# Optimization experiments

Measured on AMD Instinct MI355X. Metric: run time of the kernel, lower is better.

## Reference

```python
import jax, jax.numpy as jnp
import numpy as np


def setup_inputs() -> dict:
    key = jax.random.key(0)
    k1, k2, k3, k4, k5 = jax.random.split(key, 5)
    B, H, W, C, F = 8, 64, 64, 256, 64
    # glorot_uniform for 1x1 conv kernels [1,1,Cin,Cout]
    def glorot(k, cin, cout):
        lim = float(np.sqrt(6.0 / (cin + cout)))
        return jax.random.uniform(k, (1, 1, cin, cout), jnp.float32, -lim, lim)
    x = jax.random.normal(k1, (B, H, W, C), dtype=jnp.float32)
    Wf = glorot(k2, C, F)
    Wg = glorot(k3, C, F)
    Wh = glorot(k4, C, C)
    Wv = glorot(k5, C, C)
    gamma = jnp.zeros((1,), dtype=jnp.float32) + 0.1  # nonzero so attention path matters
    return {"x": x, "Wf": Wf, "Wg": Wg, "Wh": Wh, "Wv": Wv, "gamma": gamma}


def reference(x, Wf, Wg, Wh, Wv, gamma):
    B, H, W, C = x.shape
    N = H * W
    # 1x1 convs are pointwise matmuls over channels
    f = jnp.einsum('bhwc,cf->bhwf', x, Wf[0, 0])   # [B,H,W,F]
    g = jnp.einsum('bhwc,cf->bhwf', x, Wg[0, 0])   # [B,H,W,F]
    h = jnp.einsum('bhwc,cd->bhwd', x, Wh[0, 0])   # [B,H,W,C]
    ff = f.reshape(B, N, -1)                        # [B,N,F]
    gf = g.reshape(B, N, -1)                        # [B,N,F]
    hf = h.reshape(B, N, C)                         # [B,N,C]
    # s[b,i,j] = ff[b,i,:] . gf[b,j,:]  (no 1/sqrt(d) scaling, as in source)
    s = jnp.einsum('bif,bjf->bij', ff, gf)          # [B,N,N]
    beta = jax.nn.softmax(s, axis=-1)
    o = jnp.einsum('bij,bjc->bic', beta, hf)        # [B,N,C]
    o = o.reshape(B, H, W, C)
    o = jnp.einsum('bhwc,cd->bhwd', o, Wv[0, 0])
    return gamma * o + x
```

## Files before the change

kernel.cpp:

```cpp
#include <hip/hip_runtime.h>

typedef _Float16 half8   __attribute__((ext_vector_type(8)));
typedef _Float16 half4_t __attribute__((ext_vector_type(4)));
typedef float    float4_t __attribute__((ext_vector_type(4)));

#define B_   8
#define N_   4096
#define C_   256
#define F_   64
#define NROW (B_ * N_)
#define OPHALF ((size_t)NROW * C_)

#if defined(__has_builtin) && __has_builtin(__builtin_amdgcn_exp2f)
#define EXP2(x) __builtin_amdgcn_exp2f(x)
#else
#define EXP2(x) exp2f(x)
#endif
#define LOG2E 1.44269504f

static __device__ __forceinline__ float4_t mfma16(half8 a, half8 b, float4_t c) {
  return __builtin_amdgcn_mfma_f32_16x16x32_f16(a, b, c, 0, 0, 0);
}

template <int CTRL>
static __device__ __forceinline__ float dpp_f(float x) {
  return __int_as_float(__builtin_amdgcn_update_dpp(
      __float_as_int(x), __float_as_int(x), CTRL, 0xF, 0xF, false));
}
static __device__ __forceinline__ float row_max16(float v) {
  v = fmaxf(v, dpp_f<0x128>(v));
  v = fmaxf(v, dpp_f<0x124>(v));
  v = fmaxf(v, dpp_f<0x122>(v));
  v = fmaxf(v, dpp_f<0x121>(v));
  return v;
}
static __device__ __forceinline__ float row_sum16(float v) {
  v += dpp_f<0x128>(v);
  v += dpp_f<0x124>(v);
  v += dpp_f<0x122>(v);
  v += dpp_f<0x121>(v);
  return v;
}

__global__ __launch_bounds__(256) void prep_whvt(const float* __restrict__ Wh,
                                                 const float* __restrict__ Wv,
                                                 _Float16* __restrict__ whvt) {
  int d = blockIdx.x;
  int c = threadIdx.x;
  const float4_t* whr = (const float4_t*)(Wh + (size_t)c * 256);
  float acc = 0.f;
#pragma unroll 8
  for (int e4 = 0; e4 < 64; ++e4) {
    float4_t w4 = whr[e4];
    acc += w4[0] * Wv[(e4 * 4 + 0) * 256 + d];
    acc += w4[1] * Wv[(e4 * 4 + 1) * 256 + d];
    acc += w4[2] * Wv[(e4 * 4 + 2) * 256 + d];
    acc += w4[3] * Wv[(e4 * 4 + 3) * 256 + d];
  }
  whvt[d * 256 + c] = (_Float16)acc;
}

__global__ __launch_bounds__(256) void prep_wfgt(const float* __restrict__ Wf,
                                                 const float* __restrict__ Wg,
                                                 _Float16* __restrict__ wfgt) {
  int n = blockIdx.x;
  int c = threadIdx.x;
  float v = (n < 64) ? Wf[c * 64 + n] * LOG2E : Wg[c * 64 + (n - 64)];
  wfgt[n * 256 + c] = (_Float16)v;
}

__global__ __launch_bounds__(256) void transpose_x(const float* __restrict__ x,
                                                   _Float16* __restrict__ xT) {
  __shared__ float tile[32][33];
  int b  = blockIdx.x >> 7;
  int n0 = (blockIdx.x & 127) << 5;
  int c0 = blockIdx.y << 5;
  int tid = threadIdx.x;
  int r  = tid >> 3;
  int cc = (tid & 7) << 2;
  const float* src = x + ((size_t)(b * N_ + n0 + r)) * C_ + c0 + cc;
  float4_t v = *(const float4_t*)src;
  tile[r][cc + 0] = v[0]; tile[r][cc + 1] = v[1];
  tile[r][cc + 2] = v[2]; tile[r][cc + 3] = v[3];
  __syncthreads();
  half4_t o;
  o[0] = (_Float16)tile[cc + 0][r];
  o[1] = (_Float16)tile[cc + 1][r];
  o[2] = (_Float16)tile[cc + 2][r];
  o[3] = (_Float16)tile[cc + 3][r];
  _Float16* dst = xT + ((size_t)(b * C_ + c0 + r)) * N_ + n0 + cc;
  *(half4_t*)dst = o;
}

__global__ __launch_bounds__(256) void fg_kernel(const float* __restrict__ x,
                                                 const _Float16* __restrict__ wfgt,
                                                 _Float16* __restrict__ f,
                                                 _Float16* __restrict__ g) {
  int tid  = threadIdx.x;
  int wave = tid >> 6, lane = tid & 63;
  int n16  = lane & 15, quad = lane >> 4;
  int row  = blockIdx.x * 64 + wave * 16 + n16;
  float4_t acc[8];
#pragma unroll
  for (int t = 0; t < 8; t++) acc[t] = (float4_t){0.f, 0.f, 0.f, 0.f};
  for (int k0 = 0; k0 < 256; k0 += 32) {
    const float* xp = x + (size_t)row * C_ + k0 + quad * 8;
    float4_t x0 = *(const float4_t*)xp;
    float4_t x1 = *(const float4_t*)(xp + 4);
    half8 af;
#pragma unroll
    for (int j = 0; j < 4; j++) { af[j] = (_Float16)x0[j]; af[4 + j] = (_Float16)x1[j]; }
#pragma unroll
    for (int t = 0; t < 8; t++) {
      half8 bf = *(const half8*)(wfgt + (size_t)(t * 16 + n16) * 256 + k0 + quad * 8);
      acc[t] = mfma16(af, bf, acc[t]);
    }
  }
  int orow = blockIdx.x * 64 + wave * 16 + quad * 4;
#pragma unroll
  for (int t = 0; t < 8; t++) {
#pragma unroll
    for (int r = 0; r < 4; r++) {
      _Float16 v = (_Float16)acc[t][r];
      int col = t * 16 + n16;
      if (t < 4) f[(size_t)(orow + r) * 64 + col] = v;
      else       g[(size_t)(orow + r) * 64 + col - 64] = v;
    }
  }
}

__global__ __launch_bounds__(256, 2) void flash_kernel(const _Float16* __restrict__ f,
                                                       const _Float16* __restrict__ g,
                                                       const _Float16* __restrict__ xT,
                                                       _Float16* __restrict__ op,
                                                       float* __restrict__ ml) {
  __shared__ _Float16 ktb2[2][64 * 64];
  __shared__ _Float16 ptb2[2][64 * 64];
  __shared__ float alpha_lds[2][64];
  __shared__ int   aflag[2][4];

  const int b   = blockIdx.x;
  const int i0  = blockIdx.y * 64;
  const int jh  = blockIdx.z;
  const int jbase = jh << 11;
  const int tid = threadIdx.x;
  const int wave = tid >> 6, lane = tid & 63;
  const int n16 = lane & 15, quad = lane >> 4;
  const int nlo = n16 & 7, nhi = n16 >> 3;

  half8 qf[2];
  {
    const _Float16* qp = f + (size_t)(b * N_ + i0 + wave * 16 + n16) * 64 + quad * 8;
    qf[0] = *(const half8*)qp;
    qf[1] = *(const half8*)(qp + 32);
  }

  float4_t o_acc[16];
#pragma unroll
  for (int t = 0; t < 16; t++) o_acc[t] = (float4_t){0.f, 0.f, 0.f, 0.f};
  float m_i[4] = {-1e30f, -1e30f, -1e30f, -1e30f};
  float l_i[4] = {0.f, 0.f, 0.f, 0.f};

  const _Float16* gbase = g + (size_t)(b * N_) * 64;
  const _Float16* xbase = xT + ((size_t)b * C_ + 64 * wave) * (size_t)N_;

  const int krow = tid >> 2;
  const int kcb  = (tid & 3) << 1;
  const int krb  = krow & 7;

  {
    const _Float16* ks = gbase + (size_t)(jbase + krow) * 64 + (kcb << 3);
    half8 k0 = *(const half8*)ks;
    half8 k1 = *(const half8*)(ks + 8);
    _Float16* kd = ktb2[0] + krow * 64;
    *(half8*)(kd + (((kcb    ) ^ krb) << 3)) = k0;
    *(half8*)(kd + (((kcb + 1) ^ krb) << 3)) = k1;
  }
  __syncthreads();

  for (int k = 0; k < 32; ++k) {
    const int j0  = jbase + (k << 6);
    const int buf = k & 1;
    const int j0n = jbase + (((k + 1) & 31) << 6);

    half8 kp0, kp1;
    {
      const _Float16* ks = gbase + (size_t)(j0n + krow) * 64 + (kcb << 3);
      kp0 = *(const half8*)ks;
      kp1 = *(const half8*)(ks + 8);
    }
    half8 vfr[8];
#pragma unroll
    for (int s = 0; s < 2; s++)
#pragma unroll
      for (int ct = 0; ct < 4; ct++)
        vfr[s * 4 + ct] = *(const half8*)(xbase + (size_t)(16 * ct + n16) * N_ +
                                          j0 + 32 * s + 8 * quad);

    float4_t s_acc[4];
#pragma unroll
    for (int t = 0; t < 4; t++) s_acc[t] = (float4_t){0.f, 0.f, 0.f, 0.f};
    {
      const _Float16* ktb = ktb2[buf];
      __builtin_amdgcn_s_setprio(1);
#pragma unroll
      for (int s = 0; s < 2; s++)
#pragma unroll
        for (int t = 0; t < 4; t++) {
          half8 bf = *(const half8*)(ktb + (16 * t + n16) * 64 +
                                     (((4 * s + quad) ^ nlo) << 3));
          s_acc[t] = mfma16(qf[s], bf, s_acc[t]);
        }
      __builtin_amdgcn_s_setprio(0);
    }

    float alpha_r[4];
#pragma unroll
    for (int r = 0; r < 4; r++) {
      float v = fmaxf(fmaxf(s_acc[0][r], s_acc[1][r]),
                      fmaxf(s_acc[2][r], s_acc[3][r]));
      v = row_max16(v);
      float mn = fmaxf(m_i[r], v);
      alpha_r[r] = EXP2(m_i[r] - mn);
      m_i[r] = mn;
    }
    {
      float am = fminf(fminf(alpha_r[0], alpha_r[1]),
                       fminf(alpha_r[2], alpha_r[3]));
      unsigned long long bm = __ballot(am < 1.0f);
      if (lane == 0) aflag[buf][wave] = (bm != 0ULL) ? 1 : 0;
    }
    _Float16* pb = ptb2[buf];
#pragma unroll
    for (int r = 0; r < 4; r++) {
      float s0 = EXP2(s_acc[0][r] - m_i[r]);
      float s1 = EXP2(s_acc[1][r] - m_i[r]);
      float s2 = EXP2(s_acc[2][r] - m_i[r]);
      float s3 = EXP2(s_acc[3][r] - m_i[r]);
      float v = row_sum16(s0 + s1 + s2 + s3);
      l_i[r] = l_i[r] * alpha_r[r] + v;
      const int row = wave * 16 + 4 * quad + r;
      const int rb  = row & 7;
      _Float16* pr = pb + row * 64 + nlo;
      pr[((nhi    ) ^ rb) << 3] = (_Float16)s0;
      pr[((nhi + 2) ^ rb) << 3] = (_Float16)s1;
      pr[((nhi + 4) ^ rb) << 3] = (_Float16)s2;
      pr[((nhi + 6) ^ rb) << 3] = (_Float16)s3;
    }
    if (n16 == 0) {
#pragma unroll
      for (int r = 0; r < 4; r++)
        alpha_lds[buf][wave * 16 + 4 * quad + r] = alpha_r[r];
    }
    {
      _Float16* kd = ktb2[buf ^ 1] + krow * 64;
      *(half8*)(kd + (((kcb    ) ^ krb) << 3)) = kp0;
      *(half8*)(kd + (((kcb + 1) ^ krb) << 3)) = kp1;
    }
    __syncthreads();

#pragma unroll
    for (int ti = 0; ti < 4; ti++) {
      if (aflag[buf][ti]) {
#pragma unroll
        for (int r = 0; r < 4; r++) {
          float al = alpha_lds[buf][ti * 16 + 4 * quad + r];
#pragma unroll
          for (int ct = 0; ct < 4; ct++) o_acc[ti * 4 + ct][r] *= al;
        }
      }
    }

    __builtin_amdgcn_s_setprio(1);
#pragma unroll
    for (int s = 0; s < 2; s++)
#pragma unroll
      for (int ti = 0; ti < 4; ti++) {
        half8 af = *(const half8*)(pb + (16 * ti + n16) * 64 +
                                   (((4 * s + quad) ^ nlo) << 3));
#pragma unroll
        for (int ct = 0; ct < 4; ct++)
          o_acc[ti * 4 + ct] = mfma16(af, vfr[s * 4 + ct], o_acc[ti * 4 + ct]);
      }
    __builtin_amdgcn_s_setprio(0);
  }

  _Float16* ob = op + (size_t)jh * OPHALF;
#pragma unroll
  for (int ti = 0; ti < 4; ti++)
#pragma unroll
    for (int r = 0; r < 4; r++) {
      size_t orow = (size_t)(b * N_ + i0 + ti * 16 + 4 * quad + r) * C_;
#pragma unroll
      for (int ct = 0; ct < 4; ct++)
        ob[orow + 64 * wave + 16 * ct + n16] = (_Float16)o_acc[ti * 4 + ct][r];
    }
  if (n16 == 0) {
#pragma unroll
    for (int r = 0; r < 4; r++) {
      int rowg = b * N_ + i0 + wave * 16 + 4 * quad + r;
      ml[(size_t)(jh * 2 + 0) * NROW + rowg] = m_i[r];
      ml[(size_t)(jh * 2 + 1) * NROW + rowg] = l_i[r];
    }
  }
}

__global__ __launch_bounds__(256) void out_kernel(const _Float16* __restrict__ op,
                                                  const float* __restrict__ ml,
                                                  const _Float16* __restrict__ whvt,
                                                  const float* __restrict__ x,
                                                  const float* __restrict__ gamma,
                                                  float* __restrict__ out) {
  int tid  = threadIdx.x;
  int wave = tid >> 6, lane = tid & 63;
  int n16  = lane & 15, quad = lane >> 4;
  int row  = blockIdx.x * 64 + wave * 16 + n16;
  float m1 = ml[row],            l1 = ml[NROW + row];
  float m2 = ml[2 * NROW + row], l2 = ml[3 * NROW + row];
  float ms = fmaxf(m1, m2);
  float u1 = EXP2(m1 - ms), u2 = EXP2(m2 - ms);
  float inv = 1.f / (l1 * u1 + l2 * u2);
  float c1 = u1 * inv, c2 = u2 * inv;
  const _Float16* o1 = op + (size_t)row * C_;
  const _Float16* o2 = o1 + OPHALF;
  float4_t acc[16];
#pragma unroll
  for (int t = 0; t < 16; t++) acc[t] = (float4_t){0.f, 0.f, 0.f, 0.f};
  for (int k0 = 0; k0 < 256; k0 += 32) {
    half8 a1 = *(const half8*)(o1 + k0 + quad * 8);
    half8 a2 = *(const half8*)(o2 + k0 + quad * 8);
    half8 af;
#pragma unroll
    for (int j = 0; j < 8; j++)
      af[j] = (_Float16)((float)a1[j] * c1 + (float)a2[j] * c2);
#pragma unroll
    for (int t = 0; t < 16; t++) {
      half8 bf = *(const half8*)(whvt + (size_t)(t * 16 + n16) * 256 + k0 + quad * 8);
      acc[t] = mfma16(af, bf, acc[t]);
    }
  }
  float gm = gamma[0];
  int orow = blockIdx.x * 64 + wave * 16 + quad * 4;
#pragma unroll
  for (int t = 0; t < 16; t++) {
#pragma unroll
    for (int r = 0; r < 4; r++) {
      size_t idx = (size_t)(orow + r) * C_ + t * 16 + n16;
      out[idx] = gm * acc[t][r] + x[idx];
    }
  }
}

extern "C" void kernel_launch(void* const* d_in, const int* in_sizes, int n_in,
                              void* d_out, int out_size, void* d_ws, size_t ws_size,
                              hipStream_t stream) {
  const float* x     = (const float*)d_in[0];
  const float* Wf    = (const float*)d_in[1];
  const float* Wg    = (const float*)d_in[2];
  const float* Wh    = (const float*)d_in[3];
  const float* Wv    = (const float*)d_in[4];
  const float* gamma = (const float*)d_in[5];
  float* out = (float*)d_out;

  char* w = (char*)d_ws;
  _Float16* whvt = (_Float16*)(w);
  _Float16* wfgt = (_Float16*)(w + 131072);
  _Float16* fb   = (_Float16*)(w + 196608);
  _Float16* gb   = (_Float16*)(w + 196608 + 4194304);
  _Float16* xT   = (_Float16*)(w + 196608 + 2 * 4194304);
  _Float16* op   = (_Float16*)(w + 196608 + 2 * 4194304 + 16777216);
  float*    ml   = (float*)   (w + 196608 + 2 * 4194304 + 16777216 + 33554432);

  hipLaunchKernelGGL(prep_whvt,  dim3(256),     dim3(256), 0, stream, Wh, Wv, whvt);
  hipLaunchKernelGGL(prep_wfgt,  dim3(128),     dim3(256), 0, stream, Wf, Wg, wfgt);
  hipLaunchKernelGGL(transpose_x,dim3(1024, 8), dim3(256), 0, stream, x, xT);
  hipLaunchKernelGGL(fg_kernel,  dim3(512),     dim3(256), 0, stream, x, wfgt, fb, gb);
  hipLaunchKernelGGL(flash_kernel, dim3(8, 64, 2), dim3(256), 0, stream, fb, gb, xT, op, ml);
  hipLaunchKernelGGL(out_kernel, dim3(512),     dim3(256), 0, stream, op, ml, whvt, x, gamma, out);
}
```

Measured before the change: 313.4 us.

## Stage K tiles via direct global-to-LDS loads, split V loads, raise occupancy

Replaces register-staged K tile copies with global_load_lds direct-to-LDS transfers issued at the top of each iteration. This frees the VGPRs that used to hold the prefetched K data and removes the explicit LDS store. Half of the V fragment loads are deferred until after the softmax, behind a sched_barrier, to lower peak register pressure. The launch bound is raised to 3 waves per EU, trading register budget for occupancy. There is a risk of spills, and the async LDS writes depend on the following barrier being enough to order them before the K tile is read.

```diff
diff --git a/kernel.cpp b/kernel.cpp
--- a/kernel.cpp
+++ b/kernel.cpp
@@ -40,6 +40,23 @@
   v += dpp_f<0x122>(v);
   v += dpp_f<0x121>(v);
   return v;
+}
+
+static __device__ __forceinline__ void stage_k(const _Float16* gsrc,
+                                               _Float16* kd,
+                                               int wave, int lane) {
+  const int srow = lane >> 3;
+  const int sblk = (lane & 7) ^ srow;
+  const _Float16* s = gsrc + (size_t)(wave * 16 + srow) * 64 + (sblk << 3);
+  _Float16* d = kd + (wave * 16) * 64;
+  __builtin_amdgcn_global_load_lds(
+      (const __attribute__((address_space(1))) unsigned int*)s,
+      (__attribute__((address_space(3))) unsigned int*)d, 16, 0, 0);
+  s += 8 * 64;
+  d += 8 * 64;
+  __builtin_amdgcn_global_load_lds(
+      (const __attribute__((address_space(1))) unsigned int*)s,
+      (__attribute__((address_space(3))) unsigned int*)d, 16, 0, 0);
 }
 
 __global__ __launch_bounds__(256) void prep_whvt(const float* __restrict__ Wh,
@@ -129,7 +146,7 @@
   }
 }
 
-__global__ __launch_bounds__(256, 2) void flash_kernel(const _Float16* __restrict__ f,
+__global__ __launch_bounds__(256, 3) void flash_kernel(const _Float16* __restrict__ f,
                                                        const _Float16* __restrict__ g,
                                                        const _Float16* __restrict__ xT,
                                                        _Float16* __restrict__ op,
@@ -164,18 +181,7 @@
   const _Float16* gbase = g + (size_t)(b * N_) * 64;
   const _Float16* xbase = xT + ((size_t)b * C_ + 64 * wave) * (size_t)N_;
 
-  const int krow = tid >> 2;
-  const int kcb  = (tid & 3) << 1;
-  const int krb  = krow & 7;
-
-  {
-    const _Float16* ks = gbase + (size_t)(jbase + krow) * 64 + (kcb << 3);
-    half8 k0 = *(const half8*)ks;
-    half8 k1 = *(const half8*)(ks + 8);
-    _Float16* kd = ktb2[0] + krow * 64;
-    *(half8*)(kd + (((kcb    ) ^ krb) << 3)) = k0;
-    *(half8*)(kd + (((kcb + 1) ^ krb) << 3)) = k1;
-  }
+  stage_k(gbase + (size_t)jbase * 64, ktb2[0], wave, lane);
   __syncthreads();
 
   for (int k = 0; k < 32; ++k) {
@@ -183,19 +189,13 @@
     const int buf = k & 1;
     const int j0n = jbase + (((k + 1) & 31) << 6);
 
-    half8 kp0, kp1;
-    {
-      const _Float16* ks = gbase + (size_t)(j0n + krow) * 64 + (kcb << 3);
-      kp0 = *(const half8*)ks;
-      kp1 = *(const half8*)(ks + 8);
-    }
+    stage_k(gbase + (size_t)j0n * 64, ktb2[buf ^ 1], wave, lane);
+
     half8 vfr[8];
 #pragma unroll
-    for (int s = 0; s < 2; s++)
-#pragma unroll
-      for (int ct = 0; ct < 4; ct++)
-        vfr[s * 4 + ct] = *(const half8*)(xbase + (size_t)(16 * ct + n16) * N_ +
-                                          j0 + 32 * s + 8 * quad);
+    for (int ct = 0; ct < 4; ct++)
+      vfr[ct] = *(const half8*)(xbase + (size_t)(16 * ct + n16) * N_ +
+                                j0 + 8 * quad);
 
     float4_t s_acc[4];
 #pragma unroll
@@ -252,11 +252,12 @@
       for (int r = 0; r < 4; r++)
         alpha_lds[buf][wave * 16 + 4 * quad + r] = alpha_r[r];
     }
-    {
-      _Float16* kd = ktb2[buf ^ 1] + krow * 64;
-      *(half8*)(kd + (((kcb    ) ^ krb) << 3)) = kp0;
-      *(half8*)(kd + (((kcb + 1) ^ krb) << 3)) = kp1;
-    }
+
+    __builtin_amdgcn_sched_barrier(0);
+#pragma unroll
+    for (int ct = 0; ct < 4; ct++)
+      vfr[4 + ct] = *(const half8*)(xbase + (size_t)(16 * ct + n16) * N_ +
+                                    j0 + 32 + 8 * quad);
     __syncthreads();
 
 #pragma unroll
```

Measured after the change: 338.6 us. +8.0%, slower.
